# Performance work log

Hardware: AMD Instinct MI355X
Metric: run time of the kernel (lower is better)

## Reference

```python
import jax, jax.numpy as jnp
import numpy as np

E, H = 1024, 16
B, N = 4, 2048
D = E // H

def setup_inputs() -> dict:
    key = jax.random.key(0)
    ks = jax.random.split(key, 5)
    s = 1.0 / np.sqrt(E)
    return {
        "x": jax.random.normal(ks[0], (B, N, E), dtype=jnp.float32),
        "Wqkv": jax.random.normal(ks[1], (E, 3 * E), dtype=jnp.float32) * s,
        "bqkv": jnp.zeros((3 * E,), dtype=jnp.float32),
        "Wproj": jax.random.normal(ks[2], (E, E), dtype=jnp.float32) * s,
        "bproj": jnp.zeros((E,), dtype=jnp.float32),
    }

def reference(x, Wqkv, bqkv, Wproj, bproj):
    b, n, e = x.shape
    qkv = x @ Wqkv + bqkv  # [b, n, 3e]
    # torch rearrange 'b n (h d qkv) -> qkv b h n d': last dim splits as (h, d, 3)
    qkv = qkv.reshape(b, n, H, D, 3)
    qkv = jnp.transpose(qkv, (4, 0, 2, 1, 3))  # [3, b, h, n, d]
    q, k, v = qkv[0], qkv[1], qkv[2]
    # NOTE: module scales by 1/sqrt(e) (full embed dim), faithfully reproduced
    att = jax.nn.softmax(jnp.einsum('bhqd,bhkd->bhqk', q, k) / jnp.sqrt(jnp.float32(E)), axis=-1)
    out = jnp.einsum('bhqk,bhkd->bhqd', att, v)  # dropout is identity in eval
    out = jnp.transpose(out, (0, 2, 1, 3)).reshape(b, n, e)  # 'b h n d -> b n (h d)'
    return out @ Wproj + bproj
```

## Files before the change

### kernel.cpp

```cpp
#include <hip/hip_runtime.h>
#include <stdint.h>

typedef unsigned short u16;
typedef __attribute__((ext_vector_type(8))) short short8;
typedef __attribute__((ext_vector_type(4))) float f32x4;

#define LOG2E 1.44269504088896340736f
#define CS (0.03125f * LOG2E)
#define BB 4
#define NN 2048
#define EE 1024
#define HH 16
#define DD 64
#define MM 8192
#define C3 3072

#if __has_builtin(__builtin_amdgcn_exp2f)
#define EXP2(x) __builtin_amdgcn_exp2f(x)
#else
#define EXP2(x) exp2f(x)
#endif

__device__ __forceinline__ u16 f2bf(float f) {
  union { float f; unsigned u; } v; v.f = f;
  unsigned r = v.u + 0x7fffu + ((v.u >> 16) & 1u);
  return (u16)(r >> 16);
}

#if __has_builtin(__builtin_amdgcn_cvt_pk_bf16_f32)
typedef __attribute__((ext_vector_type(2))) __bf16 bf16x2;
__device__ __forceinline__ unsigned pk2(float a, float b) {
  union { bf16x2 v; unsigned u; } c;
  c.v = __builtin_amdgcn_cvt_pk_bf16_f32(a, b);
  return c.u;
}
#else
__device__ __forceinline__ unsigned pk2(float a, float b) {
  union { float f; unsigned u; } x, y; x.f = a; y.f = b;
  return ((x.u + 0x8000u) >> 16) | ((y.u + 0x8000u) & 0xffff0000u);
}
#endif

__device__ __forceinline__ void async16(const void* g, void* l) {
  __builtin_amdgcn_global_load_lds((const __attribute__((address_space(1))) void*)g,
                                   (__attribute__((address_space(3))) void*)l,
                                   16, 0, 0);
}


__global__ void cast_x_kernel(const float* __restrict__ x, u16* __restrict__ xb) {
  int i = (blockIdx.x * 256 + threadIdx.x) * 4;
  float4 v = *(const float4*)(x + i);
  u16 o0 = f2bf(v.x), o1 = f2bf(v.y), o2 = f2bf(v.z), o3 = f2bf(v.w);
  ushort4 o; o.x = o0; o.y = o1; o.z = o2; o.w = o3;
  *(ushort4*)(xb + i) = o;
}

__global__ void transpose_cast(const float* __restrict__ W, u16* __restrict__ Wt,
                               int ncols, int permute) {
  __shared__ float tile[32][33];
  const int c0 = blockIdx.x * 32, k0 = blockIdx.y * 32;
  const int tx = threadIdx.x & 31, ty = threadIdx.x >> 5;
#pragma unroll
  for (int r = 0; r < 32; r += 8)
    tile[ty + r][tx] = W[(size_t)(k0 + ty + r) * ncols + c0 + tx];
  __syncthreads();
#pragma unroll
  for (int r = 0; r < 32; r += 8) {
    int c = c0 + ty + r;
    int cp = c;
    if (permute) {
      int t = c % 3, hh = c / 192, d = (c / 3) % 64;
      cp = t * 1024 + hh * 64 + d;
    }
    Wt[(size_t)cp * EE + k0 + tx] = f2bf(tile[tx][ty + r]);
  }
}

__global__ void perm_bias(const float* __restrict__ bq, float* __restrict__ bp) {
  int c = blockIdx.x * 256 + threadIdx.x;
  if (c < C3) {
    int t = c % 3, hh = c / 192, d = (c / 3) % 64;
    bp[t * 1024 + hh * 64 + d] = bq[c];
  }
}


template <int KDIM>
__device__ __forceinline__ void gemm_core(const u16* __restrict__ A, const u16* __restrict__ Bt,
                                          int m0, int n0, u16* As, u16* Bs, f32x4 acc[4][4]) {
  const int tid = threadIdx.x;
  const int lane = tid & 63, wave = tid >> 6;
  const int q = lane >> 4, r16 = lane & 15;
  const int wrow = (wave >> 1) * 64, wcol = (wave & 1) * 64;
#pragma unroll
  for (int i = 0; i < 4; i++)
#pragma unroll
    for (int j = 0; j < 4; j++) acc[i][j] = (f32x4){0.f, 0.f, 0.f, 0.f};

  for (int k0 = 0; k0 < KDIM; k0 += 32) {
#pragma unroll
    for (int i = 0; i < 2; i++) {
      int chunk = i * 256 + tid;
      async16(A + (size_t)(m0 + (chunk >> 2)) * KDIM + k0 + (chunk & 3) * 8, &As[chunk * 8]);
      async16(Bt + (size_t)(n0 + (chunk >> 2)) * KDIM + k0 + (chunk & 3) * 8, &Bs[chunk * 8]);
    }
    __syncthreads();
    short8 af[4], bf[4];
#pragma unroll
    for (int i = 0; i < 4; i++)
      af[i] = *(const short8*)&As[(wrow + i * 16 + r16) * 32 + q * 8];
#pragma unroll
    for (int i = 0; i < 4; i++)
      bf[i] = *(const short8*)&Bs[(wcol + i * 16 + r16) * 32 + q * 8];
#pragma unroll
    for (int i = 0; i < 4; i++)
#pragma unroll
      for (int j = 0; j < 4; j++)
        acc[i][j] = __builtin_amdgcn_mfma_f32_16x16x32_bf16(af[i], bf[j], acc[i][j], 0, 0, 0);
    __syncthreads();
  }
}

__global__ __launch_bounds__(256) void gemm_qkv(const u16* __restrict__ Xb, const u16* __restrict__ Wt,
                                                const float* __restrict__ bqp, u16* __restrict__ Qb,
                                                u16* __restrict__ Kb, u16* __restrict__ Vt) {
  __shared__ __align__(16) u16 As[128 * 32];
  __shared__ __align__(16) u16 Bs[128 * 32];
  f32x4 acc[4][4];
  const int m0 = blockIdx.y * 128, n0 = blockIdx.x * 128;
  gemm_core<EE>(Xb, Wt, m0, n0, As, Bs, acc);
  const int tid = threadIdx.x, lane = tid & 63, wave = tid >> 6;
  const int q = lane >> 4, r16 = lane & 15;
  const int wrow = (wave >> 1) * 64, wcol = (wave & 1) * 64;
  const int t = (n0 + wcol) >> 10;
  const int b = (m0 + wrow) >> 11;
#pragma unroll
  for (int ci = 0; ci < 4; ci++) {
    const int cp = n0 + wcol + ci * 16 + r16;
    const float bias = bqp[cp];
    const int hh = (cp >> 6) & 15, d = cp & 63;
    if (t == 0) {
#pragma unroll
      for (int ri = 0; ri < 4; ri++)
#pragma unroll
        for (int r = 0; r < 4; r++) {
          const int m = m0 + wrow + ri * 16 + q * 4 + r;
          Qb[((size_t)(b * 16 + hh) * 2048 + (m & 2047)) * 64 + d] = f2bf((acc[ri][ci][r] + bias) * CS);
        }
    } else if (t == 1) {
#pragma unroll
      for (int ri = 0; ri < 4; ri++)
#pragma unroll
        for (int r = 0; r < 4; r++) {
          const int m = m0 + wrow + ri * 16 + q * 4 + r;
          Kb[((size_t)(b * 16 + hh) * 2048 + (m & 2047)) * 64 + d] = f2bf(acc[ri][ci][r] + bias);
        }
    } else {
#pragma unroll
      for (int ri = 0; ri < 4; ri++) {
        const int nb = (m0 + wrow + ri * 16 + q * 4) & 2047;
        ushort4 w;
        w.x = f2bf(acc[ri][ci][0] + bias);
        w.y = f2bf(acc[ri][ci][1] + bias);
        w.z = f2bf(acc[ri][ci][2] + bias);
        w.w = f2bf(acc[ri][ci][3] + bias);
        *(ushort4*)&Vt[((size_t)(b * 16 + hh) * 64 + d) * 2048 + nb] = w;
      }
    }
  }
}

__global__ __launch_bounds__(256) void gemm_proj(const u16* __restrict__ Ob, const u16* __restrict__ Wt,
                                                 const float* __restrict__ bp, float* __restrict__ out) {
  __shared__ __align__(16) u16 As[128 * 32];
  __shared__ __align__(16) u16 Bs[128 * 32];
  f32x4 acc[4][4];
  const int m0 = blockIdx.y * 128, n0 = blockIdx.x * 128;
  gemm_core<EE>(Ob, Wt, m0, n0, As, Bs, acc);
  const int tid = threadIdx.x, lane = tid & 63, wave = tid >> 6;
  const int q = lane >> 4, r16 = lane & 15;
  const int wrow = (wave >> 1) * 64, wcol = (wave & 1) * 64;
#pragma unroll
  for (int ci = 0; ci < 4; ci++) {
    const int col = n0 + wcol + ci * 16 + r16;
    const float bias = bp[col];
#pragma unroll
    for (int ri = 0; ri < 4; ri++)
#pragma unroll
      for (int r = 0; r < 4; r++) {
        const int m = m0 + wrow + ri * 16 + q * 4 + r;
        out[(size_t)m * EE + col] = acc[ri][ci][r] + bias;
      }
  }
}

__global__ __launch_bounds__(256, 3) void attn_kernel(const u16* __restrict__ Qg, const u16* __restrict__ Kg,
                                                      const u16* __restrict__ Vg, u16* __restrict__ Ob) {
  __shared__ __align__(16) u16 Ps[10240];
  __shared__ __align__(16) u16 Kd[2][4096];
  __shared__ __align__(16) u16 Vd[2][4096];
  const int tid = threadIdx.x, lane = tid & 63, wave = tid >> 6;
  const int q = lane >> 4, r16 = lane & 15;
  const int id = blockIdx.x + 16 * blockIdx.y;
  const int g = id & 7, s = id >> 3;
  const int bh = g * 8 + (s >> 4);
  const int q0 = (s & 15) * 128;
  const u16* Qp = Qg + ((size_t)bh * NN + q0) * DD;
  const u16* Kp = Kg + (size_t)bh * NN * DD;
  const u16* Vp = Vg + (size_t)bh * DD * NN;

  short8 qf[2][2];
#pragma unroll
  for (int nj = 0; nj < 2; nj++)
#pragma unroll
    for (int ks = 0; ks < 2; ks++)
      qf[nj][ks] = *(const short8*)(Qp + (wave * 32 + nj * 16 + r16) * 64 + ks * 32 + q * 8);

#pragma unroll
  for (int i = 0; i < 2; i++) {
    int c = i * 256 + tid;
    int ks = c >> 8, rem = c & 255, row = rem >> 2, k8 = rem & 3;
    async16(Kp + row * 64 + ks * 32 + k8 * 8, &Kd[0][c * 8]);
  }
#pragma unroll
  for (int i = 0; i < 2; i++) {
    int c = i * 256 + tid;
    int ks = c >> 8, rem = c & 255, d = rem >> 2, k8 = rem & 3;
    async16(Vp + d * NN + ks * 32 + k8 * 8, &Vd[0][c * 8]);
  }
  __syncthreads();

  f32x4 o[2][4];
  f32x4 ol[2];
#pragma unroll
  for (int i = 0; i < 2; i++) {
    ol[i] = (f32x4){0.f, 0.f, 0.f, 0.f};
#pragma unroll
    for (int j = 0; j < 4; j++) o[i][j] = (f32x4){0.f, 0.f, 0.f, 0.f};
  }
  const short8 ones = {16256, 16256, 16256, 16256, 16256, 16256, 16256, 16256};
  u16* Pw = Ps + wave * 2560;

  for (int j = 0; j < 32; j++) {
    const int buf = j & 1;
    if (j < 31) {
      const u16* Kt_ = Kp + (j + 1) * 64 * 64;
#pragma unroll
      for (int i = 0; i < 2; i++) {
        int c = i * 256 + tid;
        int ks = c >> 8, rem = c & 255, row = rem >> 2, k8 = rem & 3;
        async16(Kt_ + row * 64 + ks * 32 + k8 * 8, &Kd[buf ^ 1][c * 8]);
      }
#pragma unroll
      for (int i = 0; i < 2; i++) {
        int c = i * 256 + tid;
        int ks = c >> 8, rem = c & 255, d = rem >> 2, k8 = rem & 3;
        async16(Vp + d * NN + (j + 1) * 64 + ks * 32 + k8 * 8, &Vd[buf ^ 1][c * 8]);
      }
    }

    f32x4 st[4][2];
#pragma unroll
    for (int mi = 0; mi < 4; mi++)
#pragma unroll
      for (int nj = 0; nj < 2; nj++) st[mi][nj] = (f32x4){0.f, 0.f, 0.f, 0.f};
#pragma unroll
    for (int ks = 0; ks < 2; ks++) {
      short8 kf[4];
#pragma unroll
      for (int mi = 0; mi < 4; mi++)
        kf[mi] = *(const short8*)&Kd[buf][ks * 2048 + (mi * 16 + r16) * 32 + q * 8];
#pragma unroll
      for (int mi = 0; mi < 4; mi++)
#pragma unroll
        for (int nj = 0; nj < 2; nj++)
          st[mi][nj] = __builtin_amdgcn_mfma_f32_16x16x32_bf16(kf[mi], qf[nj][ks], st[mi][nj], 0, 0, 0);
    }

#pragma unroll
    for (int mi = 0; mi < 4; mi++)
#pragma unroll
      for (int nj = 0; nj < 2; nj++) {
        float p0 = EXP2(st[mi][nj][0]);
        float p1 = EXP2(st[mi][nj][1]);
        float p2 = EXP2(st[mi][nj][2]);
        float p3 = EXP2(st[mi][nj][3]);
        uint2 w; w.x = pk2(p0, p1); w.y = pk2(p2, p3);
        const int rowl = nj * 16 + r16;
        *(uint2*)&Pw[(mi >> 1) * 1280 + rowl * 40 + (mi & 1) * 16 + q * 4] = w;
      }

#pragma unroll
    for (int kp = 0; kp < 2; kp++) {
      short8 af[2], vf[4];
#pragma unroll
      for (int ri = 0; ri < 2; ri++)
        af[ri] = *(const short8*)&Pw[kp * 1280 + (ri * 16 + r16) * 40 + q * 8];
#pragma unroll
      for (int ci = 0; ci < 4; ci++)
        vf[ci] = *(const short8*)&Vd[buf][kp * 2048 + (ci * 16 + r16) * 32 + q * 8];
#pragma unroll
      for (int ri = 0; ri < 2; ri++) {
#pragma unroll
        for (int ci = 0; ci < 4; ci++)
          o[ri][ci] = __builtin_amdgcn_mfma_f32_16x16x32_bf16(af[ri], vf[ci], o[ri][ci], 0, 0, 0);
        ol[ri] = __builtin_amdgcn_mfma_f32_16x16x32_bf16(af[ri], ones, ol[ri], 0, 0, 0);
      }
    }

    __syncthreads();
  }

  const int b = bh >> 4, h = bh & 15;
#pragma unroll
  for (int ri = 0; ri < 2; ri++)
#pragma unroll
    for (int r = 0; r < 4; r++) {
      const float inv = 1.0f / ol[ri][r];
      const int n = q0 + wave * 32 + ri * 16 + q * 4 + r;
#pragma unroll
      for (int ci = 0; ci < 4; ci++) {
        const int d = ci * 16 + r16;
        Ob[((size_t)(b * NN + n)) * EE + h * 64 + d] = f2bf(o[ri][ci][r] * inv);
      }
    }
}


extern "C" void kernel_launch(void* const* d_in, const int* in_sizes, int n_in,
                              void* d_out, int out_size, void* d_ws, size_t ws_size,
                              hipStream_t stream) {
  const float* x     = (const float*)d_in[0];
  const float* Wqkv  = (const float*)d_in[1];
  const float* bqkv  = (const float*)d_in[2];
  const float* Wproj = (const float*)d_in[3];
  const float* bproj = (const float*)d_in[4];
  float* out = (float*)d_out;
  char* ws = (char*)d_ws;

  u16* Xb     = (u16*)(ws);
  u16* Ob     = Xb;
  u16* Qb     = (u16*)(ws + (size_t)(16 << 20));
  u16* Kb     = (u16*)(ws + (size_t)(32 << 20));
  u16* Vt     = (u16*)(ws + (size_t)(48 << 20));
  u16* WqkvT  = (u16*)(ws + (size_t)(64 << 20));
  u16* WprojT = (u16*)(ws + (size_t)(72 << 20));
  float* bqp  = (float*)(ws + (size_t)(76 << 20));

  cast_x_kernel<<<8192, 256, 0, stream>>>(x, Xb);
  transpose_cast<<<dim3(96, 32), 256, 0, stream>>>(Wqkv, WqkvT, C3, 1);
  transpose_cast<<<dim3(32, 32), 256, 0, stream>>>(Wproj, WprojT, EE, 0);
  perm_bias<<<12, 256, 0, stream>>>(bqkv, bqp);
  gemm_qkv<<<dim3(24, 64), 256, 0, stream>>>(Xb, WqkvT, bqp, Qb, Kb, Vt);
  attn_kernel<<<dim3(16, 64), 256, 0, stream>>>(Qb, Kb, Vt, Ob);
  gemm_proj<<<dim3(8, 64), 256, 0, stream>>>(Ob, WprojT, bproj, out);
}
```

Baseline: 299.4 us.

## Keep attention P in registers via permuted V layout and fuse prep kernels

Removes the per-wave LDS staging of the softmax probabilities in attention. The V^T columns are stored in a permuted order so that the QK^T MFMA output registers can be fed directly as the A operand of the PV MFMA. Freeing that LDS allows occupancy to rise from 3 to 4 blocks per CU. The x cast and both weight transpose kernels are merged into one launch, and the bias permutation kernel is dropped by indexing the original bias directly in the epilogue. Correctness depends on the permutation exactly matching the MFMA register layout.

```diff
diff --git a/kernel.cpp b/kernel.cpp
--- a/kernel.cpp
+++ b/kernel.cpp
@@ -47,19 +47,29 @@
                                    16, 0, 0);
 }
 
-
-__global__ void cast_x_kernel(const float* __restrict__ x, u16* __restrict__ xb) {
-  int i = (blockIdx.x * 256 + threadIdx.x) * 4;
-  float4 v = *(const float4*)(x + i);
-  u16 o0 = f2bf(v.x), o1 = f2bf(v.y), o2 = f2bf(v.z), o3 = f2bf(v.w);
-  ushort4 o; o.x = o0; o.y = o1; o.z = o2; o.w = o3;
-  *(ushort4*)(xb + i) = o;
-}
-
-__global__ void transpose_cast(const float* __restrict__ W, u16* __restrict__ Wt,
-                               int ncols, int permute) {
+__device__ __forceinline__ int vperm(int t) {
+  return (t & 0x23) | ((t & 8) << 1) | ((t & 4) << 1) | ((t & 16) >> 2);
+}
+
+__global__ __launch_bounds__(256) void prep_kernel(const float* __restrict__ x, u16* __restrict__ xb,
+                                                   const float* __restrict__ Wqkv, u16* __restrict__ WqkvT,
+                                                   const float* __restrict__ Wproj, u16* __restrict__ WprojT) {
   __shared__ float tile[32][33];
-  const int c0 = blockIdx.x * 32, k0 = blockIdx.y * 32;
+  const int bid = blockIdx.x;
+  if (bid < 8192) {
+    int i = (bid * 256 + threadIdx.x) * 4;
+    float4 v = *(const float4*)(x + i);
+    ushort4 o; o.x = f2bf(v.x); o.y = f2bf(v.y); o.z = f2bf(v.z); o.w = f2bf(v.w);
+    *(ushort4*)(xb + i) = o;
+    return;
+  }
+  const int permute = bid < 11264 ? 1 : 0;
+  const float* W = permute ? Wqkv : Wproj;
+  u16* Wt = permute ? WqkvT : WprojT;
+  const int ncols = permute ? C3 : EE;
+  const int t = permute ? bid - 8192 : bid - 11264;
+  const int nbx = permute ? 96 : 32;
+  const int c0 = (t % nbx) * 32, k0 = (t / nbx) * 32;
   const int tx = threadIdx.x & 31, ty = threadIdx.x >> 5;
 #pragma unroll
   for (int r = 0; r < 32; r += 8)
@@ -70,18 +80,10 @@
     int c = c0 + ty + r;
     int cp = c;
     if (permute) {
-      int t = c % 3, hh = c / 192, d = (c / 3) % 64;
-      cp = t * 1024 + hh * 64 + d;
+      int tt = c % 3, hh = c / 192, d = (c / 3) % 64;
+      cp = tt * 1024 + hh * 64 + d;
     }
     Wt[(size_t)cp * EE + k0 + tx] = f2bf(tile[tx][ty + r]);
-  }
-}
-
-__global__ void perm_bias(const float* __restrict__ bq, float* __restrict__ bp) {
-  int c = blockIdx.x * 256 + threadIdx.x;
-  if (c < C3) {
-    int t = c % 3, hh = c / 192, d = (c / 3) % 64;
-    bp[t * 1024 + hh * 64 + d] = bq[c];
   }
 }
 
@@ -123,7 +125,7 @@
 }
 
 __global__ __launch_bounds__(256) void gemm_qkv(const u16* __restrict__ Xb, const u16* __restrict__ Wt,
-                                                const float* __restrict__ bqp, u16* __restrict__ Qb,
+                                                const float* __restrict__ bqkv, u16* __restrict__ Qb,
                                                 u16* __restrict__ Kb, u16* __restrict__ Vt) {
   __shared__ __align__(16) u16 As[128 * 32];
   __shared__ __align__(16) u16 Bs[128 * 32];
@@ -138,8 +140,8 @@
 #pragma unroll
   for (int ci = 0; ci < 4; ci++) {
     const int cp = n0 + wcol + ci * 16 + r16;
-    const float bias = bqp[cp];
     const int hh = (cp >> 6) & 15, d = cp & 63;
+    const float bias = bqkv[hh * 192 + d * 3 + t];
     if (t == 0) {
 #pragma unroll
       for (int ri = 0; ri < 4; ri++)
@@ -160,12 +162,13 @@
 #pragma unroll
       for (int ri = 0; ri < 4; ri++) {
         const int nb = (m0 + wrow + ri * 16 + q * 4) & 2047;
+        const int ns = (nb & ~63) + vperm(nb & 63);
         ushort4 w;
         w.x = f2bf(acc[ri][ci][0] + bias);
         w.y = f2bf(acc[ri][ci][1] + bias);
         w.z = f2bf(acc[ri][ci][2] + bias);
         w.w = f2bf(acc[ri][ci][3] + bias);
-        *(ushort4*)&Vt[((size_t)(b * 16 + hh) * 64 + d) * 2048 + nb] = w;
+        *(ushort4*)&Vt[((size_t)(b * 16 + hh) * 64 + d) * 2048 + ns] = w;
       }
     }
   }
@@ -195,9 +198,8 @@
   }
 }
 
-__global__ __launch_bounds__(256, 3) void attn_kernel(const u16* __restrict__ Qg, const u16* __restrict__ Kg,
+__global__ __launch_bounds__(256, 4) void attn_kernel(const u16* __restrict__ Qg, const u16* __restrict__ Kg,
                                                       const u16* __restrict__ Vg, u16* __restrict__ Ob) {
-  __shared__ __align__(16) u16 Ps[10240];
   __shared__ __align__(16) u16 Kd[2][4096];
   __shared__ __align__(16) u16 Vd[2][4096];
   const int tid = threadIdx.x, lane = tid & 63, wave = tid >> 6;
@@ -240,7 +242,6 @@
     for (int j = 0; j < 4; j++) o[i][j] = (f32x4){0.f, 0.f, 0.f, 0.f};
   }
   const short8 ones = {16256, 16256, 16256, 16256, 16256, 16256, 16256, 16256};
-  u16* Pw = Ps + wave * 2560;
 
   for (int j = 0; j < 32; j++) {
     const int buf = j & 1;
@@ -278,6 +279,7 @@
           st[mi][nj] = __builtin_amdgcn_mfma_f32_16x16x32_bf16(kf[mi], qf[nj][ks], st[mi][nj], 0, 0, 0);
     }
 
+    uint2 pka[4][2];
 #pragma unroll
     for (int mi = 0; mi < 4; mi++)
 #pragma unroll
@@ -286,26 +288,27 @@
         float p1 = EXP2(st[mi][nj][1]);
         float p2 = EXP2(st[mi][nj][2]);
         float p3 = EXP2(st[mi][nj][3]);
-        uint2 w; w.x = pk2(p0, p1); w.y = pk2(p2, p3);
-        const int rowl = nj * 16 + r16;
-        *(uint2*)&Pw[(mi >> 1) * 1280 + rowl * 40 + (mi & 1) * 16 + q * 4] = w;
+        pka[mi][nj].x = pk2(p0, p1);
+        pka[mi][nj].y = pk2(p2, p3);
       }
 
 #pragma unroll
     for (int kp = 0; kp < 2; kp++) {
-      short8 af[2], vf[4];
-#pragma unroll
-      for (int ri = 0; ri < 2; ri++)
-        af[ri] = *(const short8*)&Pw[kp * 1280 + (ri * 16 + r16) * 40 + q * 8];
+      short8 vf[4];
 #pragma unroll
       for (int ci = 0; ci < 4; ci++)
         vf[ci] = *(const short8*)&Vd[buf][kp * 2048 + (ci * 16 + r16) * 32 + q * 8];
 #pragma unroll
       for (int ri = 0; ri < 2; ri++) {
+        union { uint4 u; short8 s; } a;
+        a.u.x = pka[2 * kp][ri].x;
+        a.u.y = pka[2 * kp][ri].y;
+        a.u.z = pka[2 * kp + 1][ri].x;
+        a.u.w = pka[2 * kp + 1][ri].y;
 #pragma unroll
         for (int ci = 0; ci < 4; ci++)
-          o[ri][ci] = __builtin_amdgcn_mfma_f32_16x16x32_bf16(af[ri], vf[ci], o[ri][ci], 0, 0, 0);
-        ol[ri] = __builtin_amdgcn_mfma_f32_16x16x32_bf16(af[ri], ones, ol[ri], 0, 0, 0);
+          o[ri][ci] = __builtin_amdgcn_mfma_f32_16x16x32_bf16(a.s, vf[ci], o[ri][ci], 0, 0, 0);
+        ol[ri] = __builtin_amdgcn_mfma_f32_16x16x32_bf16(a.s, ones, ol[ri], 0, 0, 0);
       }
     }
 
@@ -346,13 +349,9 @@
   u16* Vt     = (u16*)(ws + (size_t)(48 << 20));
   u16* WqkvT  = (u16*)(ws + (size_t)(64 << 20));
   u16* WprojT = (u16*)(ws + (size_t)(72 << 20));
-  float* bqp  = (float*)(ws + (size_t)(76 << 20));
-
-  cast_x_kernel<<<8192, 256, 0, stream>>>(x, Xb);
-  transpose_cast<<<dim3(96, 32), 256, 0, stream>>>(Wqkv, WqkvT, C3, 1);
-  transpose_cast<<<dim3(32, 32), 256, 0, stream>>>(Wproj, WprojT, EE, 0);
-  perm_bias<<<12, 256, 0, stream>>>(bqkv, bqp);
-  gemm_qkv<<<dim3(24, 64), 256, 0, stream>>>(Xb, WqkvT, bqp, Qb, Kb, Vt);
+
+  prep_kernel<<<12288, 256, 0, stream>>>(x, Xb, Wqkv, WqkvT, Wproj, WprojT);
+  gemm_qkv<<<dim3(24, 64), 256, 0, stream>>>(Xb, WqkvT, bqkv, Qb, Kb, Vt);
   attn_kernel<<<dim3(16, 64), 256, 0, stream>>>(Qb, Kb, Vt, Ob);
   gemm_proj<<<dim3(8, 64), 256, 0, stream>>>(Ob, WprojT, bproj, out);
 }
```

New measurement: 272.4 us. 9.0% less time.
